# Optimization experiments

Measured on AMD Instinct MI355X. Metric: run time of the kernel, lower is better.

The kernel has to match this reference:

```python
import jax, jax.numpy as jnp
import numpy as np

MIN_VAL = float(-2**32 + 1)  # sentinel used to exclude padded cells from top-k
KS = (1, 3, -1)              # default ks; -1 means masked mean pooling


def setup_inputs() -> dict:
    key = jax.random.key(0)
    k1, k2, k3 = jax.random.split(key, 3)
    B, X, Y, C = 32, 128, 256, 64
    inp_mm = jax.random.normal(k1, (B, X, Y, C), dtype=jnp.float32)
    # prefix (padding) masks: ones up to a random valid length
    x_lens = jax.random.randint(k2, (B,), 1, X + 1)
    y_lens = jax.random.randint(k3, (B,), 4, Y + 1)  # >= 4 so top-3 is meaningful
    x_mask = (jnp.arange(X)[None, :] < x_lens[:, None]).astype(jnp.float32)
    y_mask = (jnp.arange(Y)[None, :] < y_lens[:, None]).astype(jnp.float32)
    return {"inp_mm": inp_mm, "x_mask": x_mask, "y_mask": y_mask}


def reference(inp_mm, x_mask, y_mask):
    # inp_mm: [B, X, Y, C]; x_mask: [B, X]; y_mask: [B, Y]
    # joint validity mask, broadcast over channels: [B, X, Y, 1]
    mask = (x_mask[:, :, None] * y_mask[:, None, :])[..., None]
    mm_min = jnp.where(mask == 0, MIN_VAL, inp_mm)   # masked with -inf-like sentinel
    mm_zero = jnp.where(mask == 0, 0.0, inp_mm)      # masked with zeros

    y_real_len = jnp.sum(y_mask, axis=1)[:, None, None]          # [B, 1, 1]
    mean_pool = jnp.sum(mm_zero, axis=2) / y_real_len            # [B, X, C]
    x_mask_exp = x_mask[:, :, None]                              # [B, X, 1]

    topk_in = jnp.transpose(mm_min, (0, 1, 3, 2))                # [B, X, C, Y]
    outs = []
    for k in KS:
        if k == -1:
            outs.append(mean_pool)  # NB: original does not re-mask mean pooling
        else:
            top_k_vals, _ = jax.lax.top_k(topk_in, k)            # [B, X, C, k]
            top_k_mean = jnp.mean(top_k_vals, axis=-1)           # [B, X, C]
            top_k_mean = jnp.where(y_real_len < k, mean_pool, top_k_mean)
            outs.append(top_k_mean * x_mask_exp)
    return jnp.stack(outs, axis=2)  # [B, X, len(KS), C]
```

## Files before the change

### kernel.cpp

```cpp
#include <hip/hip_runtime.h>

#define B_ 32
#define X_ 128
#define Y_ 256
#define C_ 64
#define BDIM 256
#define MIN_VALF -4294967295.0f

__device__ __forceinline__ void insert3(float& m1, float& m2, float& m3, float v) {
    float hi1 = fmaxf(m1, v);
    float lo1 = fminf(m1, v);
    m1 = hi1;
    float hi2 = fmaxf(m2, lo1);
    float lo2 = fminf(m2, lo1);
    m2 = hi2;
    m3 = fmaxf(m3, lo2);
}

__global__ __launch_bounds__(BDIM) void topk_pool_kernel(
    const float* __restrict__ inp,
    const float* __restrict__ xmask,
    const float* __restrict__ ymask,
    float* __restrict__ out)
{
    const int tid  = threadIdx.x;
    const int lane = tid & 63;
    const int wv   = tid >> 6;

    const int w = (blockIdx.x * 1997) & (B_ * X_ - 1);
    const int b = w >> 7;
    const int x = w & (X_ - 1);

    __shared__ float lds[4 * 16 * 16];

    const float xm = xmask[b * X_ + x];
    const float* ym = ymask + b * Y_;
    const float y0v = ym[lane];
    const float y1v = ym[lane + 64];
    const float y2v = ym[lane + 128];
    const float y3v = ym[lane + 192];

    float* orow = out + (size_t)w * (3 * C_);

    if (xm == 0.0f) {
        if (wv == 0) {
            orow[lane]       = 0.0f;
            orow[64 + lane]  = 0.0f;
            orow[128 + lane] = 0.0f;
        }
        return;
    }

    float ysum = y0v + y1v + y2v + y3v;
    #pragma unroll
    for (int off = 32; off > 0; off >>= 1) ysum += __shfl_xor(ysum, off);
    const int   ylen    = (int)(ysum + 0.5f);
    const float inv_len = 1.0f / ysum;

    const int c0   = (lane & 15) << 2;
    const int yofs = lane >> 4;

    float m1[4], m2[4], m3[4], s[4];
    #pragma unroll
    for (int j = 0; j < 4; ++j) {
        m1[j] = MIN_VALF; m2[j] = MIN_VALF; m3[j] = MIN_VALF; s[j] = 0.0f;
    }

    const float* base = inp + (size_t)(b * X_ + x) * (Y_ * C_) + c0;
    const int y_lo = wv * 64;
    const int y0   = y_lo + yofs;

    if (y_lo < ylen) {
        if (y_lo + 64 <= ylen) {
            float4 v[16];
            #pragma unroll
            for (int i = 0; i < 16; ++i)
                v[i] = *reinterpret_cast<const float4*>(base + (size_t)(y0 + 4 * i) * C_);
            #pragma unroll
            for (int i = 0; i < 16; ++i) {
                float vv[4] = {v[i].x, v[i].y, v[i].z, v[i].w};
                #pragma unroll
                for (int j = 0; j < 4; ++j) {
                    s[j] += vv[j];
                    insert3(m1[j], m2[j], m3[j], vv[j]);
                }
            }
        } else {
            float4 v[16];
            #pragma unroll
            for (int i = 0; i < 16; ++i) {
                const int yr = y0 + 4 * i;
                const int yc = (yr < ylen) ? yr : (ylen - 1);
                v[i] = *reinterpret_cast<const float4*>(base + (size_t)yc * C_);
            }
            #pragma unroll
            for (int i = 0; i < 16; ++i) {
                const bool live = (y0 + 4 * i) < ylen;
                float vv[4] = {v[i].x, v[i].y, v[i].z, v[i].w};
                #pragma unroll
                for (int j = 0; j < 4; ++j) {
                    const float vs = live ? vv[j] : 0.0f;
                    const float vt = live ? vv[j] : MIN_VALF;
                    s[j] += vs;
                    insert3(m1[j], m2[j], m3[j], vt);
                }
            }
        }
    }

    #pragma unroll
    for (int step = 0; step < 2; ++step) {
        const int msk = 16 << step;
        #pragma unroll
        for (int j = 0; j < 4; ++j) {
            float o1 = __shfl_xor(m1[j], msk);
            float o2 = __shfl_xor(m2[j], msk);
            float o3 = __shfl_xor(m3[j], msk);
            float os = __shfl_xor(s[j],  msk);
            s[j] += os;
            insert3(m1[j], m2[j], m3[j], o1);
            insert3(m1[j], m2[j], m3[j], o2);
            insert3(m1[j], m2[j], m3[j], o3);
        }
    }

    if (yofs == 0) {
        float* dst = &lds[(wv * 16 + (lane & 15)) * 16];
        *reinterpret_cast<float4*>(dst +  0) = make_float4(m1[0], m1[1], m1[2], m1[3]);
        *reinterpret_cast<float4*>(dst +  4) = make_float4(m2[0], m2[1], m2[2], m2[3]);
        *reinterpret_cast<float4*>(dst +  8) = make_float4(m3[0], m3[1], m3[2], m3[3]);
        *reinterpret_cast<float4*>(dst + 12) = make_float4(s[0],  s[1],  s[2],  s[3]);
    }
    __syncthreads();

    if (wv == 0) {
        const int ch = lane, lg = ch >> 2, e = ch & 3;
        float M1 = MIN_VALF, M2 = MIN_VALF, M3 = MIN_VALF, S = 0.0f;
        #pragma unroll
        for (int q = 0; q < 4; ++q) {
            const float* src = &lds[(q * 16 + lg) * 16];
            float a = src[e], bb = src[4 + e], c = src[8 + e], d = src[12 + e];
            S += d;
            insert3(M1, M2, M3, a);
            insert3(M1, M2, M3, bb);
            insert3(M1, M2, M3, c);
        }
        const float mean = S * inv_len;
        const float top1 = M1 * xm;
        const float top3 = ((ylen >= 3) ? (M1 + M2 + M3) * (1.0f / 3.0f) : mean) * xm;
        orow[ch]       = top1;
        orow[64 + ch]  = top3;
        orow[128 + ch] = mean;
    }
}

extern "C" void kernel_launch(void* const* d_in, const int* in_sizes, int n_in,
                              void* d_out, int out_size, void* d_ws, size_t ws_size,
                              hipStream_t stream) {
    const float* inp   = (const float*)d_in[0];
    const float* xmask = (const float*)d_in[1];
    const float* ymask = (const float*)d_in[2];
    float* out = (float*)d_out;

    const int grid = B_ * X_;
    topk_pool_kernel<<<grid, BDIM, 0, stream>>>(inp, xmask, ymask, out);
}
```

Baseline: 20.63 us.

## Use persistent blocks with atomic work queues partitioned by block group

Replaces the one-block-per-(b,x)-row launch with 1024 persistent blocks. Each block pulls row indices from one of four atomic counters in workspace, which is zeroed by a memset before launch. The aim is to balance the uneven work from variable-length masks and to cut per-block launch overhead. In exchange it adds a memset, an atomic round trip and two barriers per item, and it removes the overlap between blocks that separate launches would give.

```diff
diff --git a/kernel.cpp b/kernel.cpp
--- a/kernel.cpp
+++ b/kernel.cpp
@@ -5,6 +5,8 @@
 #define Y_ 256
 #define C_ 64
 #define BDIM 256
+#define NPART 4
+#define ITEMS_PER_PART (B_ * X_ / NPART)
 #define MIN_VALF -4294967295.0f
 
 __device__ __forceinline__ void insert3(float& m1, float& m2, float& m3, float v) {
@@ -21,136 +23,145 @@
     const float* __restrict__ inp,
     const float* __restrict__ xmask,
     const float* __restrict__ ymask,
-    float* __restrict__ out)
+    float* __restrict__ out,
+    unsigned* __restrict__ queues)
 {
     const int tid  = threadIdx.x;
     const int lane = tid & 63;
     const int wv   = tid >> 6;
-
-    const int w = (blockIdx.x * 1997) & (B_ * X_ - 1);
-    const int b = w >> 7;
-    const int x = w & (X_ - 1);
-
-    __shared__ float lds[4 * 16 * 16];
-
-    const float xm = xmask[b * X_ + x];
-    const float* ym = ymask + b * Y_;
-    const float y0v = ym[lane];
-    const float y1v = ym[lane + 64];
-    const float y2v = ym[lane + 128];
-    const float y3v = ym[lane + 192];
-
-    float* orow = out + (size_t)w * (3 * C_);
-
-    if (xm == 0.0f) {
-        if (wv == 0) {
-            orow[lane]       = 0.0f;
-            orow[64 + lane]  = 0.0f;
-            orow[128 + lane] = 0.0f;
-        }
-        return;
-    }
-
-    float ysum = y0v + y1v + y2v + y3v;
-    #pragma unroll
-    for (int off = 32; off > 0; off >>= 1) ysum += __shfl_xor(ysum, off);
-    const int   ylen    = (int)(ysum + 0.5f);
-    const float inv_len = 1.0f / ysum;
-
     const int c0   = (lane & 15) << 2;
     const int yofs = lane >> 4;
 
-    float m1[4], m2[4], m3[4], s[4];
-    #pragma unroll
-    for (int j = 0; j < 4; ++j) {
-        m1[j] = MIN_VALF; m2[j] = MIN_VALF; m3[j] = MIN_VALF; s[j] = 0.0f;
-    }
+    const int part   = blockIdx.x & (NPART - 1);
+    unsigned* q      = queues + part * 64;
+    const int gbase  = part * ITEMS_PER_PART;
 
-    const float* base = inp + (size_t)(b * X_ + x) * (Y_ * C_) + c0;
-    const int y_lo = wv * 64;
-    const int y0   = y_lo + yofs;
+    __shared__ float lds[4 * 16 * 16];
+    __shared__ int   g_sh;
 
-    if (y_lo < ylen) {
-        if (y_lo + 64 <= ylen) {
-            float4 v[16];
-            #pragma unroll
-            for (int i = 0; i < 16; ++i)
-                v[i] = *reinterpret_cast<const float4*>(base + (size_t)(y0 + 4 * i) * C_);
-            #pragma unroll
-            for (int i = 0; i < 16; ++i) {
-                float vv[4] = {v[i].x, v[i].y, v[i].z, v[i].w};
+    for (;;) {
+        __syncthreads();
+        if (tid == 0) g_sh = (int)atomicAdd(q, 1u);
+        __syncthreads();
+        const int idx = g_sh;
+        if (idx >= ITEMS_PER_PART) return;
+
+        const int w = ((gbase + idx) * 1997) & (B_ * X_ - 1);
+        const int b = w >> 7;
+        const int x = w & (X_ - 1);
+
+        const float xm  = xmask[b * X_ + x];
+        const float* ym = ymask + b * Y_;
+        const float y0v = ym[lane];
+        const float y1v = ym[lane + 64];
+        const float y2v = ym[lane + 128];
+        const float y3v = ym[lane + 192];
+
+        float* orow = out + (size_t)w * (3 * C_);
+
+        if (xm == 0.0f) {
+            if (wv == 0) {
+                orow[lane]       = 0.0f;
+                orow[64 + lane]  = 0.0f;
+                orow[128 + lane] = 0.0f;
+            }
+            continue;
+        }
+
+        float ysum = y0v + y1v + y2v + y3v;
+        #pragma unroll
+        for (int off = 32; off > 0; off >>= 1) ysum += __shfl_xor(ysum, off);
+        const int   ylen    = (int)(ysum + 0.5f);
+        const float inv_len = 1.0f / ysum;
+
+        float m1[4], m2[4], m3[4], s[4];
+        #pragma unroll
+        for (int j = 0; j < 4; ++j) {
+            m1[j] = MIN_VALF; m2[j] = MIN_VALF; m3[j] = MIN_VALF; s[j] = 0.0f;
+        }
+
+        const float* base = inp + ((size_t)w << 14) + c0;
+        const int y_lo = wv * 64;
+        const int y0   = y_lo + yofs;
+
+        if (y_lo < ylen) {
+            if (y_lo + 64 <= ylen) {
+                float4 v[16];
                 #pragma unroll
-                for (int j = 0; j < 4; ++j) {
-                    s[j] += vv[j];
-                    insert3(m1[j], m2[j], m3[j], vv[j]);
+                for (int i = 0; i < 16; ++i)
+                    v[i] = *reinterpret_cast<const float4*>(base + (size_t)(y0 + 4 * i) * C_);
+                #pragma unroll
+                for (int i = 0; i < 16; ++i) {
+                    float vv[4] = {v[i].x, v[i].y, v[i].z, v[i].w};
+                    #pragma unroll
+                    for (int j = 0; j < 4; ++j) {
+                        s[j] += vv[j];
+                        insert3(m1[j], m2[j], m3[j], vv[j]);
+                    }
                 }
-            }
-        } else {
-            float4 v[16];
-            #pragma unroll
-            for (int i = 0; i < 16; ++i) {
-                const int yr = y0 + 4 * i;
-                const int yc = (yr < ylen) ? yr : (ylen - 1);
-                v[i] = *reinterpret_cast<const float4*>(base + (size_t)yc * C_);
-            }
-            #pragma unroll
-            for (int i = 0; i < 16; ++i) {
-                const bool live = (y0 + 4 * i) < ylen;
-                float vv[4] = {v[i].x, v[i].y, v[i].z, v[i].w};
+            } else {
+                float4 v[16];
                 #pragma unroll
-                for (int j = 0; j < 4; ++j) {
-                    const float vs = live ? vv[j] : 0.0f;
-                    const float vt = live ? vv[j] : MIN_VALF;
-                    s[j] += vs;
-                    insert3(m1[j], m2[j], m3[j], vt);
+                for (int i = 0; i < 16; ++i) {
+                    const int yr = y0 + 4 * i;
+                    const int yc = (yr < ylen) ? yr : (ylen - 1);
+                    v[i] = *reinterpret_cast<const float4*>(base + (size_t)yc * C_);
+                }
+                #pragma unroll
+                for (int i = 0; i < 16; ++i) {
+                    const bool live = (y0 + 4 * i) < ylen;
+                    float vv[4] = {v[i].x, v[i].y, v[i].z, v[i].w};
+                    #pragma unroll
+                    for (int j = 0; j < 4; ++j) {
+                        s[j] += live ? vv[j] : 0.0f;
+                        insert3(m1[j], m2[j], m3[j], live ? vv[j] : MIN_VALF);
+                    }
                 }
             }
         }
-    }
 
-    #pragma unroll
-    for (int step = 0; step < 2; ++step) {
-        const int msk = 16 << step;
         #pragma unroll
-        for (int j = 0; j < 4; ++j) {
-            float o1 = __shfl_xor(m1[j], msk);
-            float o2 = __shfl_xor(m2[j], msk);
-            float o3 = __shfl_xor(m3[j], msk);
-            float os = __shfl_xor(s[j],  msk);
-            s[j] += os;
-            insert3(m1[j], m2[j], m3[j], o1);
-            insert3(m1[j], m2[j], m3[j], o2);
-            insert3(m1[j], m2[j], m3[j], o3);
+        for (int step = 0; step < 2; ++step) {
+            const int msk = 16 << step;
+            #pragma unroll
+            for (int j = 0; j < 4; ++j) {
+                float o1 = __shfl_xor(m1[j], msk);
+                float o2 = __shfl_xor(m2[j], msk);
+                float o3 = __shfl_xor(m3[j], msk);
+                float os = __shfl_xor(s[j],  msk);
+                s[j] += os;
+                insert3(m1[j], m2[j], m3[j], o1);
+                insert3(m1[j], m2[j], m3[j], o2);
+                insert3(m1[j], m2[j], m3[j], o3);
+            }
         }
-    }
 
-    if (yofs == 0) {
-        float* dst = &lds[(wv * 16 + (lane & 15)) * 16];
-        *reinterpret_cast<float4*>(dst +  0) = make_float4(m1[0], m1[1], m1[2], m1[3]);
-        *reinterpret_cast<float4*>(dst +  4) = make_float4(m2[0], m2[1], m2[2], m2[3]);
-        *reinterpret_cast<float4*>(dst +  8) = make_float4(m3[0], m3[1], m3[2], m3[3]);
-        *reinterpret_cast<float4*>(dst + 12) = make_float4(s[0],  s[1],  s[2],  s[3]);
-    }
-    __syncthreads();
+        if (yofs == 0) {
+            float* dst = &lds[(wv * 16 + (lane & 15)) * 16];
+            *reinterpret_cast<float4*>(dst +  0) = make_float4(m1[0], m1[1], m1[2], m1[3]);
+            *reinterpret_cast<float4*>(dst +  4) = make_float4(m2[0], m2[1], m2[2], m2[3]);
+            *reinterpret_cast<float4*>(dst +  8) = make_float4(m3[0], m3[1], m3[2], m3[3]);
+            *reinterpret_cast<float4*>(dst + 12) = make_float4(s[0],  s[1],  s[2],  s[3]);
+        }
+        __syncthreads();
 
-    if (wv == 0) {
-        const int ch = lane, lg = ch >> 2, e = ch & 3;
-        float M1 = MIN_VALF, M2 = MIN_VALF, M3 = MIN_VALF, S = 0.0f;
-        #pragma unroll
-        for (int q = 0; q < 4; ++q) {
-            const float* src = &lds[(q * 16 + lg) * 16];
-            float a = src[e], bb = src[4 + e], c = src[8 + e], d = src[12 + e];
-            S += d;
-            insert3(M1, M2, M3, a);
-            insert3(M1, M2, M3, bb);
-            insert3(M1, M2, M3, c);
+        if (wv == 0) {
+            const int lg = lane >> 2, e = lane & 3;
+            float M1 = MIN_VALF, M2 = MIN_VALF, M3 = MIN_VALF, S = 0.0f;
+            #pragma unroll
+            for (int qq = 0; qq < 4; ++qq) {
+                const float* src = &lds[(qq * 16 + lg) * 16];
+                float a = src[e], bb = src[4 + e], c = src[8 + e], d = src[12 + e];
+                S += d;
+                insert3(M1, M2, M3, a);
+                insert3(M1, M2, M3, bb);
+                insert3(M1, M2, M3, c);
+            }
+            const float mean = S * inv_len;
+            orow[lane]       = M1 * xm;
+            orow[64 + lane]  = ((ylen >= 3) ? (M1 + M2 + M3) * (1.0f / 3.0f) : mean) * xm;
+            orow[128 + lane] = mean;
         }
-        const float mean = S * inv_len;
-        const float top1 = M1 * xm;
-        const float top3 = ((ylen >= 3) ? (M1 + M2 + M3) * (1.0f / 3.0f) : mean) * xm;
-        orow[ch]       = top1;
-        orow[64 + ch]  = top3;
-        orow[128 + ch] = mean;
     }
 }
 
@@ -161,7 +172,10 @@
     const float* xmask = (const float*)d_in[1];
     const float* ymask = (const float*)d_in[2];
     float* out = (float*)d_out;
+    unsigned* queues = (unsigned*)d_ws;
 
-    const int grid = B_ * X_;
-    topk_pool_kernel<<<grid, BDIM, 0, stream>>>(inp, xmask, ymask, out);
+    hipMemsetAsync(d_ws, 0, NPART * 64 * sizeof(unsigned), stream);
+
+    const int grid = 1024;
+    topk_pool_kernel<<<grid, BDIM, 0, stream>>>(inp, xmask, ymask, out, queues);
 }
```

New measurement: 30.76 us. 49.1% more time.
